# Kernel tuning notes

Measured on AMD Instinct MI355X. Metric: run time of the kernel, lower is better.

Reference implementation:

```python
import jax, jax.numpy as jnp
import numpy as np

D_MODEL = 1024
N_HEADS = 16
HEAD_DIM = D_MODEL // N_HEADS  # 64
TOP_K = 64
EPS = 1e-12  # matches F.normalize eps


def setup_inputs() -> dict:
    key = jax.random.key(0)
    ks = jax.random.split(key, 6)
    s = 0.02
    def w(k):
        return jax.random.normal(k, (D_MODEL, D_MODEL), jnp.float32) * s
    zb = jnp.zeros((D_MODEL,), jnp.float32)
    # x: (B, T, d_model); T must equal d_model (see compress_proj constraint)
    x = jax.random.normal(ks[0], (2, 1024, D_MODEL), jnp.float32)
    return {
        "x": x,
        "Wq": w(ks[1]), "bq": zb,
        "Wk": w(ks[2]), "bk": zb,
        "Wv": w(ks[3]), "bv": zb,
        "Wo": w(ks[4]), "bo": zb,
        "Wc": w(ks[5]), "bc": zb,  # compress_proj (applied along time axis)
    }


def _l2norm(a):
    n = jnp.linalg.norm(a, axis=-1, keepdims=True)
    return a / jnp.maximum(n, EPS)


def reference(x, Wq, bq, Wk, bk, Wv, bv, Wo, bo, Wc, bc):
    B, T, Dm = x.shape
    H, hd = N_HEADS, HEAD_DIM

    def proj(W, b):
        return (x @ W.T + b).reshape(B, T, H, hd).transpose(0, 2, 1, 3)  # (B,H,T,hd)

    Q = proj(Wq, bq)
    K = proj(Wk, bk)
    V = proj(Wv, bv)

    # compress_kv with compress_ratio=1: compress_proj acts on the (transposed)
    # time axis, so K_comp[b,h,c,d] = sum_t K[b,h,t,d] * Wc[c,t] + bc[c]
    K_comp = jnp.einsum('bhtd,ct->bhcd', K, Wc) + bc[None, None, :, None]
    V_comp = jnp.einsum('bhtd,ct->bhcd', V, Wc) + bc[None, None, :, None]

    # lightning indexer: cosine similarity + top-k over compressed slots
    sim = jnp.einsum('bhtd,bhcd->bhtc', _l2norm(Q), _l2norm(K_comp))
    topk_idx = jax.lax.top_k(sim, TOP_K)[1]  # (B,H,T,K)

    bi = jnp.arange(B)[:, None, None, None]
    hi = jnp.arange(H)[None, :, None, None]
    K_sel = K_comp[bi, hi, topk_idx]  # (B,H,T,K,hd)
    V_sel = V_comp[bi, hi, topk_idx]

    scores = jnp.einsum('bhtd,bhtkd->bhtk', Q, K_sel) / float(np.sqrt(hd))
    attn = jax.nn.softmax(scores, axis=-1)
    out = jnp.einsum('bhtk,bhtkd->bhtd', attn, V_sel)  # (B,H,T,hd)
    out = out.transpose(0, 2, 1, 3).reshape(B, T, Dm)
    return out @ Wo.T + bo
```

## Files before the change

kernel.cpp:

```cpp
#include <hip/hip_runtime.h>
#include <type_traits>


#define DEVI __device__ __forceinline__

constexpr int Tn = 1024;
constexpr int Cn = 1024;
constexpr int Hn = 16;

typedef short bf16x8 __attribute__((ext_vector_type(8)));
typedef float f32x4 __attribute__((ext_vector_type(4)));
typedef double f64x4 __attribute__((ext_vector_type(4)));

DEVI int wsumi(int v)   { for (int m = 1; m < 64; m <<= 1) v += __shfl_xor(v, m); return v; }
DEVI int wmini(int v)   { for (int m = 1; m < 64; m <<= 1) { int o = __shfl_xor(v, m); v = o < v ? o : v; } return v; }
DEVI float wfmax(float v){ for (int m = 1; m < 64; m <<= 1) v = fmaxf(v, __shfl_xor(v, m)); return v; }
DEVI float wfsum(float v){ for (int m = 1; m < 64; m <<= 1) v += __shfl_xor(v, m); return v; }

DEVI unsigned long long mapd(double x) {
  unsigned long long b = (unsigned long long)__double_as_longlong(x);
  return (b >> 63) ? ~b : (b | 0x8000000000000000ull);
}

DEVI unsigned short f2bf_rne(float x) {
  unsigned u = __float_as_uint(x);
  u += 0x7fffu + ((u >> 16) & 1u);
  return (unsigned short)(u >> 16);
}
struct BfPair { short hi, lo; };
DEVI BfPair split2(float x) {
  unsigned short h = f2bf_rne(x);
  float hf = __uint_as_float(((unsigned)h) << 16);
  BfPair r;
  r.hi = (short)h;
  r.lo = (short)f2bf_rne(x - hf);
  return r;
}

template <typename OUTT, bool BTRANS, int BIASMODE, bool SIM>
__global__ __launch_bounds__(256) void f64sel_k(
    const float* __restrict__ A, const float* __restrict__ B,
    const float* __restrict__ bias, OUTT* __restrict__ C,
    int Kd, int lda, int ldb, int ldc,
    long long zB, long long zC, int group_base)
{
  __shared__ float As[32][72];
  __shared__ float Bs[32][72];

  size_t offA = 0, offB = 0, offC = 0;
  if (SIM) {
    int pair = group_base + (int)blockIdx.z;
    int bb = pair >> 4, hh = pair & 15;
    offA = ((size_t)bb * Tn) * (size_t)lda + (size_t)hh * 64;
    offB = ((size_t)bb * Cn) * (size_t)ldb + (size_t)hh * 64;
    offC = (size_t)blockIdx.z * (size_t)Tn * (size_t)ldc;
  } else {
    offB = (size_t)blockIdx.z * (size_t)zB;
    offC = (size_t)blockIdx.z * (size_t)zC;
  }
  const float* Ab = A + offA;
  const float* Bb = B + offB;
  OUTT* Cb = C + offC;

  const int tid = threadIdx.x;
  const int lane = tid & 63, w = tid >> 6;
  const int wr = w >> 1, wc = w & 1;
  const int l15 = lane & 15, l4 = lane >> 4;
  const int m0 = blockIdx.y * 64, n0 = blockIdx.x * 64;

  f64x4 zz = {0.0, 0.0, 0.0, 0.0};
  f64x4 p1 = __builtin_amdgcn_mfma_f64_16x16x4f64(1.0, (double)l15, zz, 0, 0, 0);
  f64x4 p2 = __builtin_amdgcn_mfma_f64_16x16x4f64((double)l15, 1.0, zz, 0, 0, 0);
  int a1 = 1, b1 = 1, c1 = 1, a2 = 1, b2 = 1, c2 = 1;
#pragma unroll
  for (int rr = 0; rr < 4; ++rr) {
    a1 &= (p1[rr] == 4.0 * l15);
    b1 &= (p1[rr] == 4.0 * (l4 * 4 + rr));
    c1 &= (p1[rr] == 4.0 * (l4 + 4 * rr));
    a2 &= (p2[rr] == 4.0 * (l4 * 4 + rr));
    b2 &= (p2[rr] == 4.0 * (l4 + 4 * rr));
    c2 &= (p2[rr] == 4.0 * l15);
  }
  a1 = __all(a1); b1 = __all(b1); c1 = __all(c1);
  a2 = __all(a2); b2 = __all(b2); c2 = __all(c2);
  int dmap = 0, useM = 1;
  if      (a1 && a2) dmap = 0;
  else if (a1 && b2) dmap = 1;
  else if (b1 && c2) dmap = 2;
  else if (c1 && c2) dmap = 3;
  else useM = 0;

  f64x4 acc[2][2];
#pragma unroll
  for (int i = 0; i < 2; ++i)
#pragma unroll
    for (int j = 0; j < 2; ++j) acc[i][j] = (f64x4){0.0, 0.0, 0.0, 0.0};

  const int sm = tid >> 2, skf = tid & 3;
  const int bkl = tid >> 4, bnf = tid & 15;

  const int nT = Kd >> 5;
  float4 a0_, a1_, b0_, b1_;
  {
    a0_ = *(const float4*)(Ab + (size_t)(m0 + sm) * lda + 4 * skf);
    a1_ = *(const float4*)(Ab + (size_t)(m0 + sm) * lda + 16 + 4 * skf);
    if (BTRANS) {
      b0_ = *(const float4*)(Bb + (size_t)(n0 + sm) * ldb + 4 * skf);
      b1_ = *(const float4*)(Bb + (size_t)(n0 + sm) * ldb + 16 + 4 * skf);
    } else {
      b0_ = *(const float4*)(Bb + (size_t)bkl * ldb + n0 + 4 * bnf);
      b1_ = *(const float4*)(Bb + (size_t)(16 + bkl) * ldb + n0 + 4 * bnf);
    }
  }

  for (int kt = 0; kt < nT; ++kt) {
    As[4 * skf + 0][sm] = a0_.x; As[4 * skf + 1][sm] = a0_.y;
    As[4 * skf + 2][sm] = a0_.z; As[4 * skf + 3][sm] = a0_.w;
    As[16 + 4 * skf + 0][sm] = a1_.x; As[16 + 4 * skf + 1][sm] = a1_.y;
    As[16 + 4 * skf + 2][sm] = a1_.z; As[16 + 4 * skf + 3][sm] = a1_.w;
    if (BTRANS) {
      Bs[4 * skf + 0][sm] = b0_.x; Bs[4 * skf + 1][sm] = b0_.y;
      Bs[4 * skf + 2][sm] = b0_.z; Bs[4 * skf + 3][sm] = b0_.w;
      Bs[16 + 4 * skf + 0][sm] = b1_.x; Bs[16 + 4 * skf + 1][sm] = b1_.y;
      Bs[16 + 4 * skf + 2][sm] = b1_.z; Bs[16 + 4 * skf + 3][sm] = b1_.w;
    } else {
      *(float4*)&Bs[bkl][4 * bnf] = b0_;
      *(float4*)&Bs[16 + bkl][4 * bnf] = b1_;
    }
    __syncthreads();

    if (kt + 1 < nT) {
      int k0 = (kt + 1) * 32;
      a0_ = *(const float4*)(Ab + (size_t)(m0 + sm) * lda + k0 + 4 * skf);
      a1_ = *(const float4*)(Ab + (size_t)(m0 + sm) * lda + k0 + 16 + 4 * skf);
      if (BTRANS) {
        b0_ = *(const float4*)(Bb + (size_t)(n0 + sm) * ldb + k0 + 4 * skf);
        b1_ = *(const float4*)(Bb + (size_t)(n0 + sm) * ldb + k0 + 16 + 4 * skf);
      } else {
        b0_ = *(const float4*)(Bb + (size_t)(k0 + bkl) * ldb + n0 + 4 * bnf);
        b1_ = *(const float4*)(Bb + (size_t)(k0 + 16 + bkl) * ldb + n0 + 4 * bnf);
      }
    }

    if (useM) {
#pragma unroll
      for (int kq = 0; kq < 8; ++kq) {
        int kk = kq * 4 + l4;
        double a0  = (double)As[kk][wr * 32 + l15];
        double a1v = (double)As[kk][wr * 32 + 16 + l15];
        double b0  = (double)Bs[kk][wc * 32 + l15];
        double b1v = (double)Bs[kk][wc * 32 + 16 + l15];
        acc[0][0] = __builtin_amdgcn_mfma_f64_16x16x4f64(a0,  b0,  acc[0][0], 0, 0, 0);
        acc[0][1] = __builtin_amdgcn_mfma_f64_16x16x4f64(a0,  b1v, acc[0][1], 0, 0, 0);
        acc[1][0] = __builtin_amdgcn_mfma_f64_16x16x4f64(a1v, b0,  acc[1][0], 0, 0, 0);
        acc[1][1] = __builtin_amdgcn_mfma_f64_16x16x4f64(a1v, b1v, acc[1][1], 0, 0, 0);
      }
    } else {
#pragma unroll
      for (int k = 0; k < 32; ++k) {
        double bv0 = (double)Bs[k][wc * 32 + l15];
        double bv1 = (double)Bs[k][wc * 32 + 16 + l15];
#pragma unroll
        for (int fr = 0; fr < 2; ++fr)
#pragma unroll
          for (int rr = 0; rr < 4; ++rr) {
            double av = (double)As[k][wr * 32 + fr * 16 + l4 * 4 + rr];
            acc[fr][0][rr] += av * bv0;
            acc[fr][1][rr] += av * bv1;
          }
      }
    }
    __syncthreads();
  }

#pragma unroll
  for (int fr = 0; fr < 2; ++fr)
#pragma unroll
    for (int fc = 0; fc < 2; ++fc)
#pragma unroll
      for (int rr = 0; rr < 4; ++rr) {
        int ri, ci;
        if (!useM || dmap == 0) { ri = l4 * 4 + rr; ci = l15; }
        else if (dmap == 1)     { ri = l4 + 4 * rr; ci = l15; }
        else if (dmap == 2)     { ri = l15; ci = l4 * 4 + rr; }
        else                    { ri = l15; ci = l4 + 4 * rr; }
        int row = m0 + wr * 32 + fr * 16 + ri;
        int col = n0 + wc * 32 + fc * 16 + ci;
        double v = acc[fr][fc][rr];
        if constexpr (std::is_same<OUTT, double>::value) {
          Cb[(size_t)row * ldc + col] = v;
        } else {
          float s = (float)v;
          float cb = (BIASMODE == 1) ? bias[col] : 0.f;
          float rb = (BIASMODE == 2) ? bias[row] : 0.f;
          ((float*)Cb)[(size_t)row * ldc + col] = s + cb + rb;
        }
      }
}

template <bool BTRANS, int BIASMODE>
__global__ __launch_bounds__(256) void mfma_gemm_k(
    const float* __restrict__ A, const float* __restrict__ B,
    const float* __restrict__ bias, float* __restrict__ C,
    int Kd, int lda, int ldb, int ldc, long long zB, long long zC)
{
  __shared__ short Ah[4 * 64 * 8];
  __shared__ short Al[4 * 64 * 8];
  __shared__ short Bh[4 * 64 * 8];
  __shared__ short Bl[4 * 64 * 8];

  const float* Bz = B + (size_t)blockIdx.z * (size_t)zB;
  float* Cz = C + (size_t)blockIdx.z * (size_t)zC;

  const int tid = threadIdx.x;
  const int lane = tid & 63, w = tid >> 6;
  const int wr = w >> 1, wc = w & 1;
  const int m0 = blockIdx.y * 64, n0 = blockIdx.x * 64;
  const int r16 = lane & 15, kg = lane >> 4;

  f32x4 acc[2][2];
#pragma unroll
  for (int i = 0; i < 2; ++i)
#pragma unroll
    for (int j = 0; j < 2; ++j) acc[i][j] = (f32x4){0.f, 0.f, 0.f, 0.f};

  const int row = tid >> 2, kseg = tid & 3;
  const int gcol = tid & 63, gks = tid >> 6;

  const int nT = Kd >> 5;
  float4 pa0, pa1, pb0, pb1;
  float gb[8];
  {
    pa0 = *(const float4*)(A + (size_t)(m0 + row) * lda + kseg * 8);
    pa1 = *(const float4*)(A + (size_t)(m0 + row) * lda + kseg * 8 + 4);
    if (BTRANS) {
      pb0 = *(const float4*)(Bz + (size_t)(n0 + row) * ldb + kseg * 8);
      pb1 = *(const float4*)(Bz + (size_t)(n0 + row) * ldb + kseg * 8 + 4);
    } else {
#pragma unroll
      for (int j = 0; j < 8; ++j)
        gb[j] = Bz[(size_t)(gks * 8 + j) * ldb + n0 + gcol];
    }
  }

  for (int kt = 0; kt < nT; ++kt) {
    {
      BfPair q0 = split2(pa0.x), q1 = split2(pa0.y), q2 = split2(pa0.z), q3 = split2(pa0.w);
      BfPair q4 = split2(pa1.x), q5 = split2(pa1.y), q6 = split2(pa1.z), q7 = split2(pa1.w);
      bf16x8 h = {q0.hi, q1.hi, q2.hi, q3.hi, q4.hi, q5.hi, q6.hi, q7.hi};
      bf16x8 l = {q0.lo, q1.lo, q2.lo, q3.lo, q4.lo, q5.lo, q6.lo, q7.lo};
      int idx = (kseg * 64 + row) * 8;
      *(bf16x8*)&Ah[idx] = h;
      *(bf16x8*)&Al[idx] = l;
    }
    if (BTRANS) {
      BfPair q0 = split2(pb0.x), q1 = split2(pb0.y), q2 = split2(pb0.z), q3 = split2(pb0.w);
      BfPair q4 = split2(pb1.x), q5 = split2(pb1.y), q6 = split2(pb1.z), q7 = split2(pb1.w);
      bf16x8 h = {q0.hi, q1.hi, q2.hi, q3.hi, q4.hi, q5.hi, q6.hi, q7.hi};
      bf16x8 l = {q0.lo, q1.lo, q2.lo, q3.lo, q4.lo, q5.lo, q6.lo, q7.lo};
      int idx = (kseg * 64 + row) * 8;
      *(bf16x8*)&Bh[idx] = h;
      *(bf16x8*)&Bl[idx] = l;
    } else {
      short hv[8], lv[8];
#pragma unroll
      for (int j = 0; j < 8; ++j) {
        BfPair p = split2(gb[j]);
        hv[j] = p.hi; lv[j] = p.lo;
      }
      bf16x8 h = {hv[0], hv[1], hv[2], hv[3], hv[4], hv[5], hv[6], hv[7]};
      bf16x8 l = {lv[0], lv[1], lv[2], lv[3], lv[4], lv[5], lv[6], lv[7]};
      int idx = (gks * 64 + gcol) * 8;
      *(bf16x8*)&Bh[idx] = h;
      *(bf16x8*)&Bl[idx] = l;
    }
    __syncthreads();

    if (kt + 1 < nT) {
      int k0 = (kt + 1) * 32;
      pa0 = *(const float4*)(A + (size_t)(m0 + row) * lda + k0 + kseg * 8);
      pa1 = *(const float4*)(A + (size_t)(m0 + row) * lda + k0 + kseg * 8 + 4);
      if (BTRANS) {
        pb0 = *(const float4*)(Bz + (size_t)(n0 + row) * ldb + k0 + kseg * 8);
        pb1 = *(const float4*)(Bz + (size_t)(n0 + row) * ldb + k0 + kseg * 8 + 4);
      } else {
#pragma unroll
        for (int j = 0; j < 8; ++j)
          gb[j] = Bz[(size_t)(k0 + gks * 8 + j) * ldb + n0 + gcol];
      }
    }

    bf16x8 ah[2], al[2], bh[2], bl[2];
#pragma unroll
    for (int f = 0; f < 2; ++f) {
      int ia = (kg * 64 + wr * 32 + f * 16 + r16) * 8;
      int ib = (kg * 64 + wc * 32 + f * 16 + r16) * 8;
      ah[f] = *(const bf16x8*)&Ah[ia];
      al[f] = *(const bf16x8*)&Al[ia];
      bh[f] = *(const bf16x8*)&Bh[ib];
      bl[f] = *(const bf16x8*)&Bl[ib];
    }
#pragma unroll
    for (int fr = 0; fr < 2; ++fr)
#pragma unroll
      for (int fc = 0; fc < 2; ++fc) {
        f32x4 c = acc[fr][fc];
        c = __builtin_amdgcn_mfma_f32_16x16x32_bf16(al[fr], bh[fc], c, 0, 0, 0);
        c = __builtin_amdgcn_mfma_f32_16x16x32_bf16(ah[fr], bl[fc], c, 0, 0, 0);
        c = __builtin_amdgcn_mfma_f32_16x16x32_bf16(ah[fr], bh[fc], c, 0, 0, 0);
        acc[fr][fc] = c;
      }
    __syncthreads();
  }

#pragma unroll
  for (int fr = 0; fr < 2; ++fr)
#pragma unroll
    for (int fc = 0; fc < 2; ++fc) {
      int col = n0 + wc * 32 + fc * 16 + r16;
      float cb = (BIASMODE == 1) ? bias[col] : 0.f;
#pragma unroll
      for (int rr = 0; rr < 4; ++rr) {
        int rw = m0 + wr * 32 + fr * 16 + kg * 4 + rr;
        float rb = (BIASMODE == 2) ? bias[rw] : 0.f;
        Cz[(size_t)rw * ldc + col] = acc[fr][fc][rr] + cb + rb;
      }
    }
}

__global__ __launch_bounds__(256) void kn_k2(const float* __restrict__ Kc,
                                             double* __restrict__ kn)
{
  int idx = (int)blockIdx.x * 256 + (int)threadIdx.x;
  int c = idx & 1023;
  int p = idx >> 10;
  int b = p >> 4, h = p & 15;
  const float* row = Kc + ((size_t)(b * 1024 + c)) * 1024 + h * 64;
  double s = 0.0;
  for (int d = 0; d < 64; ++d) { double v = (double)row[d]; s += v * v; }
  kn[(size_t)p * 1024 + c] = 1.0 / fmax(sqrt(s), 1e-12);
}

__global__ __launch_bounds__(256) void topk_attn_k(
    const double* __restrict__ dotb, const double* __restrict__ kn,
    const float* __restrict__ Vc, float* __restrict__ attnout, int group_base)
{
  __shared__ int sC[4][64];
  __shared__ float sD[4][64];

  const int lane = threadIdx.x & 63, wv = threadIdx.x >> 6;
  const int g = (int)blockIdx.x >> 8;
  const int t = ((int)blockIdx.x & 255) * 4 + wv;
  const int pair = group_base + g;
  const int bb = pair >> 4, hh = pair & 15;

  const double* drow = dotb + ((size_t)g * Tn + t) * (size_t)Cn;
  const double* knr  = kn + ((size_t)(bb * Hn + hh)) * Cn;

  double dv[16];
  unsigned long long u[16];
#pragma unroll
  for (int j = 0; j < 8; ++j) {
    double2 dd = *(const double2*)(drow + j * 128 + 2 * lane);
    double2 kk = *(const double2*)(knr  + j * 128 + 2 * lane);
    dv[2 * j] = dd.x; dv[2 * j + 1] = dd.y;
    u[2 * j]     = mapd(dd.x * kk.x);
    u[2 * j + 1] = mapd(dd.y * kk.y);
  }
  unsigned hi[16];
#pragma unroll
  for (int i = 0; i < 16; ++i) hi[i] = (unsigned)(u[i] >> 32);

  unsigned TH = 0;
  for (int bit = 31; bit >= 0; --bit) {
    unsigned Tc = TH | (1u << bit);
    int c = 0;
#pragma unroll
    for (int i = 0; i < 16; ++i) c += (hi[i] >= Tc);
    if (wsumi(c) >= 64) TH = Tc;
  }
  int mhi = 0;
#pragma unroll
  for (int i = 0; i < 16; ++i) mhi += (hi[i] > TH);
  mhi = wsumi(mhi);
  const int need1 = 64 - mhi;
  unsigned TL = 0;
  for (int bit = 31; bit >= 0; --bit) {
    unsigned Tc = TL | (1u << bit);
    int c = 0;
#pragma unroll
    for (int i = 0; i < 16; ++i) c += (hi[i] == TH && (unsigned)u[i] >= Tc);
    if (wsumi(c) >= need1) TL = Tc;
  }
  const unsigned long long V64 = ((unsigned long long)TH << 32) | TL;

  int base = 0;
#pragma unroll
  for (int i = 0; i < 16; ++i) {
    const int cix = 128 * (i >> 1) + 2 * lane + (i & 1);
    bool sel = (u[i] > V64);
    unsigned long long mk = __ballot(sel);
    if (sel) {
      int r = __popcll(mk & ((1ull << lane) - 1ull));
      sC[wv][base + r] = cix;
      sD[wv][base + r] = (float)dv[i];
    }
    base += __popcll(mk);
  }
  const int need = 64 - base;
  unsigned taken = 0;
  for (int r = 0; r < need; ++r) {
    int mn = 0x7fffffff;
#pragma unroll
    for (int i = 0; i < 16; ++i) {
      int cix = 128 * (i >> 1) + 2 * lane + (i & 1);
      if (u[i] == V64 && !((taken >> i) & 1u)) mn = mn < cix ? mn : cix;
    }
    mn = wmini(mn);
#pragma unroll
    for (int i = 0; i < 16; ++i) {
      int cix = 128 * (i >> 1) + 2 * lane + (i & 1);
      if (u[i] == V64 && !((taken >> i) & 1u) && cix == mn) {
        taken |= 1u << i;
        sC[wv][base + r] = mn;
        sD[wv][base + r] = (float)dv[i];
      }
    }
  }
  __syncthreads();

  int ck = sC[wv][lane];
  float sc = sD[wv][lane] * 0.125f;
  float mx = wfmax(sc);
  float w = expf(sc - mx);
  float sw = wfsum(w);
  w /= sw;

  const float* Vb = Vc + (size_t)bb * ((size_t)Cn * 1024) + hh * 64 + lane;
  float acc = 0.f;
#pragma unroll 4
  for (int k = 0; k < 64; ++k) {
    int c = __shfl(ck, k);
    float wk = __shfl(w, k);
    acc = fmaf(wk, Vb[(size_t)c * 1024], acc);
  }
  attnout[((size_t)(bb * Tn + t)) * 1024 + hh * 64 + lane] = acc;
}

extern "C" void kernel_launch(void* const* d_in, const int* in_sizes, int n_in,
                              void* d_out, int out_size, void* d_ws, size_t ws_size,
                              hipStream_t stream)
{
  const float* x  = (const float*)d_in[0];
  const float* Wq = (const float*)d_in[1];
  const float* bq = (const float*)d_in[2];
  const float* Wk = (const float*)d_in[3];
  const float* bk = (const float*)d_in[4];
  const float* Wv = (const float*)d_in[5];
  const float* bv = (const float*)d_in[6];
  const float* Wo = (const float*)d_in[7];
  const float* bo = (const float*)d_in[8];
  const float* Wc = (const float*)d_in[9];
  const float* bc = (const float*)d_in[10];
  float* out = (float*)d_out;

  const size_t NE = (size_t)2048 * 1024;
  const size_t M1 = (size_t)1024 * 1024;
  float* Q   = (float*)d_ws;
  float* Kf  = Q + NE;
  float* Vf  = Kf + NE;
  float* Kc  = Vf + NE;
  float* Vc  = Kc + NE;
  float* at  = Vc + NE;
  double* kn = (double*)(at + NE);
  double* tail = kn + 32768;

  const size_t fixedB = 6 * NE * 4 + 32768 * 8;
  const size_t dotPairB = (size_t)Tn * Cn * 8;
  if (ws_size < fixedB) return;

  size_t rem = ws_size - fixedB;
  double* dotp; int G;
  if      (rem >= 8 * dotPairB) { G = 8; dotp = tail; }
  else if (rem >= 4 * dotPairB) { G = 4; dotp = tail; }
  else if (rem >= 2 * dotPairB) { G = 2; dotp = tail; }
  else { G = 2; dotp = (double*)Kf; }

  dim3 blk(256, 1, 1);

  f64sel_k<float, true, 1, false><<<dim3(16, 32, 1), blk, 0, stream>>>(
      x, Wq, bq, Q, 1024, 1024, 1024, 1024, 0, 0, 0);
  f64sel_k<float, true, 1, false><<<dim3(16, 32, 1), blk, 0, stream>>>(
      x, Wk, bk, Kf, 1024, 1024, 1024, 1024, 0, 0, 0);
  mfma_gemm_k<true, 1><<<dim3(16, 32, 1), blk, 0, stream>>>(
      x, Wv, bv, Vf, 1024, 1024, 1024, 1024, 0, 0);

  f64sel_k<float, false, 2, false><<<dim3(16, 16, 2), blk, 0, stream>>>(
      Wc, Kf, bc, Kc, 1024, 1024, 1024, 1024, (long long)M1, (long long)M1, 0);
  mfma_gemm_k<false, 2><<<dim3(16, 16, 2), blk, 0, stream>>>(
      Wc, Vf, bc, Vc, 1024, 1024, 1024, 1024, (long long)M1, (long long)M1);

  kn_k2<<<dim3(128), blk, 0, stream>>>(Kc, kn);

  for (int gb = 0; gb < 32; gb += G) {
    f64sel_k<double, true, 0, true><<<dim3(16, 16, G), blk, 0, stream>>>(
        Q, Kc, nullptr, dotp, 64, 1024, 1024, 1024, 0, 0, gb);
    topk_attn_k<<<dim3(256 * G), blk, 0, stream>>>(dotp, kn, Vc, at, gb);
  }

  mfma_gemm_k<true, 1><<<dim3(16, 32, 1), blk, 0, stream>>>(
      at, Wo, bo, out, 1024, 1024, 1024, 1024, 0, 0);
}
```

Measured before the change: 856.8 us.

## Double-buffer GEMM LDS tiles, batch Q/K projections, enlarge similarity group size

Both GEMM kernels now use two shared-memory buffers. The next tile is written to the idle buffer after the compute step, so each k-iteration needs one barrier instead of two. The Q and K projections are merged into a single launch through a new mode that picks weights, bias and output from blockIdx.z. The similarity/top-k group size can now reach 32 pairs when the workspace allows, which cuts the number of launch pairs. In exchange, LDS use doubles, which may lower occupancy, and the larger groups need more workspace.

```diff
diff --git a/kernel.cpp b/kernel.cpp
--- a/kernel.cpp
+++ b/kernel.cpp
@@ -37,30 +37,32 @@
   return r;
 }
 
-template <typename OUTT, bool BTRANS, int BIASMODE, bool SIM>
+template <typename OUTT, bool BTRANS, int BIASMODE, int MODE>
 __global__ __launch_bounds__(256) void f64sel_k(
     const float* __restrict__ A, const float* __restrict__ B,
-    const float* __restrict__ bias, OUTT* __restrict__ C,
+    const float* __restrict__ Bx, const float* __restrict__ bias,
+    const float* __restrict__ biasx, OUTT* __restrict__ C, OUTT* __restrict__ Cx,
     int Kd, int lda, int ldb, int ldc,
     long long zB, long long zC, int group_base)
 {
-  __shared__ float As[32][72];
-  __shared__ float Bs[32][72];
-
-  size_t offA = 0, offB = 0, offC = 0;
-  if (SIM) {
+  __shared__ float As[2][32][72];
+  __shared__ float Bs[2][32][72];
+
+  const float* Ab = A;
+  const float* Bb = B;
+  OUTT* Cb = C;
+  if (MODE == 1) {
     int pair = group_base + (int)blockIdx.z;
     int bb = pair >> 4, hh = pair & 15;
-    offA = ((size_t)bb * Tn) * (size_t)lda + (size_t)hh * 64;
-    offB = ((size_t)bb * Cn) * (size_t)ldb + (size_t)hh * 64;
-    offC = (size_t)blockIdx.z * (size_t)Tn * (size_t)ldc;
+    Ab = A + ((size_t)bb * Tn) * (size_t)lda + (size_t)hh * 64;
+    Bb = B + ((size_t)bb * Cn) * (size_t)ldb + (size_t)hh * 64;
+    Cb = C + (size_t)blockIdx.z * (size_t)Tn * (size_t)ldc;
+  } else if (MODE == 0) {
+    Bb = B + (size_t)blockIdx.z * (size_t)zB;
+    Cb = C + (size_t)blockIdx.z * (size_t)zC;
   } else {
-    offB = (size_t)blockIdx.z * (size_t)zB;
-    offC = (size_t)blockIdx.z * (size_t)zC;
-  }
-  const float* Ab = A + offA;
-  const float* Bb = B + offB;
-  OUTT* Cb = C + offC;
+    if (blockIdx.z == 1) { Bb = Bx; bias = biasx; Cb = Cx; }
+  }
 
   const int tid = threadIdx.x;
   const int lane = tid & 63, w = tid >> 6;
@@ -101,55 +103,50 @@
 
   const int nT = Kd >> 5;
   float4 a0_, a1_, b0_, b1_;
-  {
-    a0_ = *(const float4*)(Ab + (size_t)(m0 + sm) * lda + 4 * skf);
-    a1_ = *(const float4*)(Ab + (size_t)(m0 + sm) * lda + 16 + 4 * skf);
+
+  auto LOADT = [&](int k0) {
+    a0_ = *(const float4*)(Ab + (size_t)(m0 + sm) * lda + k0 + 4 * skf);
+    a1_ = *(const float4*)(Ab + (size_t)(m0 + sm) * lda + k0 + 16 + 4 * skf);
     if (BTRANS) {
-      b0_ = *(const float4*)(Bb + (size_t)(n0 + sm) * ldb + 4 * skf);
-      b1_ = *(const float4*)(Bb + (size_t)(n0 + sm) * ldb + 16 + 4 * skf);
+      b0_ = *(const float4*)(Bb + (size_t)(n0 + sm) * ldb + k0 + 4 * skf);
+      b1_ = *(const float4*)(Bb + (size_t)(n0 + sm) * ldb + k0 + 16 + 4 * skf);
     } else {
-      b0_ = *(const float4*)(Bb + (size_t)bkl * ldb + n0 + 4 * bnf);
-      b1_ = *(const float4*)(Bb + (size_t)(16 + bkl) * ldb + n0 + 4 * bnf);
-    }
-  }
+      b0_ = *(const float4*)(Bb + (size_t)(k0 + bkl) * ldb + n0 + 4 * bnf);
+      b1_ = *(const float4*)(Bb + (size_t)(k0 + 16 + bkl) * ldb + n0 + 4 * bnf);
+    }
+  };
+  auto WRITET = [&](int buf) {
+    As[buf][4 * skf + 0][sm] = a0_.x; As[buf][4 * skf + 1][sm] = a0_.y;
+    As[buf][4 * skf + 2][sm] = a0_.z; As[buf][4 * skf + 3][sm] = a0_.w;
+    As[buf][16 + 4 * skf + 0][sm] = a1_.x; As[buf][16 + 4 * skf + 1][sm] = a1_.y;
+    As[buf][16 + 4 * skf + 2][sm] = a1_.z; As[buf][16 + 4 * skf + 3][sm] = a1_.w;
+    if (BTRANS) {
+      Bs[buf][4 * skf + 0][sm] = b0_.x; Bs[buf][4 * skf + 1][sm] = b0_.y;
+      Bs[buf][4 * skf + 2][sm] = b0_.z; Bs[buf][4 * skf + 3][sm] = b0_.w;
+      Bs[buf][16 + 4 * skf + 0][sm] = b1_.x; Bs[buf][16 + 4 * skf + 1][sm] = b1_.y;
+      Bs[buf][16 + 4 * skf + 2][sm] = b1_.z; Bs[buf][16 + 4 * skf + 3][sm] = b1_.w;
+    } else {
+      *(float4*)&Bs[buf][bkl][4 * bnf] = b0_;
+      *(float4*)&Bs[buf][16 + bkl][4 * bnf] = b1_;
+    }
+  };
+
+  LOADT(0);
+  WRITET(0);
+  __syncthreads();
 
   for (int kt = 0; kt < nT; ++kt) {
-    As[4 * skf + 0][sm] = a0_.x; As[4 * skf + 1][sm] = a0_.y;
-    As[4 * skf + 2][sm] = a0_.z; As[4 * skf + 3][sm] = a0_.w;
-    As[16 + 4 * skf + 0][sm] = a1_.x; As[16 + 4 * skf + 1][sm] = a1_.y;
-    As[16 + 4 * skf + 2][sm] = a1_.z; As[16 + 4 * skf + 3][sm] = a1_.w;
-    if (BTRANS) {
-      Bs[4 * skf + 0][sm] = b0_.x; Bs[4 * skf + 1][sm] = b0_.y;
-      Bs[4 * skf + 2][sm] = b0_.z; Bs[4 * skf + 3][sm] = b0_.w;
-      Bs[16 + 4 * skf + 0][sm] = b1_.x; Bs[16 + 4 * skf + 1][sm] = b1_.y;
-      Bs[16 + 4 * skf + 2][sm] = b1_.z; Bs[16 + 4 * skf + 3][sm] = b1_.w;
-    } else {
-      *(float4*)&Bs[bkl][4 * bnf] = b0_;
-      *(float4*)&Bs[16 + bkl][4 * bnf] = b1_;
-    }
-    __syncthreads();
-
-    if (kt + 1 < nT) {
-      int k0 = (kt + 1) * 32;
-      a0_ = *(const float4*)(Ab + (size_t)(m0 + sm) * lda + k0 + 4 * skf);
-      a1_ = *(const float4*)(Ab + (size_t)(m0 + sm) * lda + k0 + 16 + 4 * skf);
-      if (BTRANS) {
-        b0_ = *(const float4*)(Bb + (size_t)(n0 + sm) * ldb + k0 + 4 * skf);
-        b1_ = *(const float4*)(Bb + (size_t)(n0 + sm) * ldb + k0 + 16 + 4 * skf);
-      } else {
-        b0_ = *(const float4*)(Bb + (size_t)(k0 + bkl) * ldb + n0 + 4 * bnf);
-        b1_ = *(const float4*)(Bb + (size_t)(k0 + 16 + bkl) * ldb + n0 + 4 * bnf);
-      }
-    }
+    const int cur = kt & 1;
+    if (kt + 1 < nT) LOADT((kt + 1) * 32);
 
     if (useM) {
 #pragma unroll
       for (int kq = 0; kq < 8; ++kq) {
         int kk = kq * 4 + l4;
-        double a0  = (double)As[kk][wr * 32 + l15];
-        double a1v = (double)As[kk][wr * 32 + 16 + l15];
-        double b0  = (double)Bs[kk][wc * 32 + l15];
-        double b1v = (double)Bs[kk][wc * 32 + 16 + l15];
+        double a0  = (double)As[cur][kk][wr * 32 + l15];
+        double a1v = (double)As[cur][kk][wr * 32 + 16 + l15];
+        double b0  = (double)Bs[cur][kk][wc * 32 + l15];
+        double b1v = (double)Bs[cur][kk][wc * 32 + 16 + l15];
         acc[0][0] = __builtin_amdgcn_mfma_f64_16x16x4f64(a0,  b0,  acc[0][0], 0, 0, 0);
         acc[0][1] = __builtin_amdgcn_mfma_f64_16x16x4f64(a0,  b1v, acc[0][1], 0, 0, 0);
         acc[1][0] = __builtin_amdgcn_mfma_f64_16x16x4f64(a1v, b0,  acc[1][0], 0, 0, 0);
@@ -158,18 +155,20 @@
     } else {
 #pragma unroll
       for (int k = 0; k < 32; ++k) {
-        double bv0 = (double)Bs[k][wc * 32 + l15];
-        double bv1 = (double)Bs[k][wc * 32 + 16 + l15];
+        double bv0 = (double)Bs[cur][k][wc * 32 + l15];
+        double bv1 = (double)Bs[cur][k][wc * 32 + 16 + l15];
 #pragma unroll
         for (int fr = 0; fr < 2; ++fr)
 #pragma unroll
           for (int rr = 0; rr < 4; ++rr) {
-            double av = (double)As[k][wr * 32 + fr * 16 + l4 * 4 + rr];
+            double av = (double)As[cur][k][wr * 32 + fr * 16 + l4 * 4 + rr];
             acc[fr][0][rr] += av * bv0;
             acc[fr][1][rr] += av * bv1;
           }
       }
     }
+
+    if (kt + 1 < nT) WRITET(cur ^ 1);
     __syncthreads();
   }
 
@@ -204,10 +203,10 @@
     const float* __restrict__ bias, float* __restrict__ C,
     int Kd, int lda, int ldb, int ldc, long long zB, long long zC)
 {
-  __shared__ short Ah[4 * 64 * 8];
-  __shared__ short Al[4 * 64 * 8];
-  __shared__ short Bh[4 * 64 * 8];
-  __shared__ short Bl[4 * 64 * 8];
+  __shared__ short Ah[2][4 * 64 * 8];
+  __shared__ short Al[2][4 * 64 * 8];
+  __shared__ short Bh[2][4 * 64 * 8];
+  __shared__ short Bl[2][4 * 64 * 8];
 
   const float* Bz = B + (size_t)blockIdx.z * (size_t)zB;
   float* Cz = C + (size_t)blockIdx.z * (size_t)zC;
@@ -230,28 +229,28 @@
   const int nT = Kd >> 5;
   float4 pa0, pa1, pb0, pb1;
   float gb[8];
-  {
-    pa0 = *(const float4*)(A + (size_t)(m0 + row) * lda + kseg * 8);
-    pa1 = *(const float4*)(A + (size_t)(m0 + row) * lda + kseg * 8 + 4);
+
+  auto LOADT = [&](int k0) {
+    pa0 = *(const float4*)(A + (size_t)(m0 + row) * lda + k0 + kseg * 8);
+    pa1 = *(const float4*)(A + (size_t)(m0 + row) * lda + k0 + kseg * 8 + 4);
     if (BTRANS) {
-      pb0 = *(const float4*)(Bz + (size_t)(n0 + row) * ldb + kseg * 8);
-      pb1 = *(const float4*)(Bz + (size_t)(n0 + row) * ldb + kseg * 8 + 4);
+      pb0 = *(const float4*)(Bz + (size_t)(n0 + row) * ldb + k0 + kseg * 8);
+      pb1 = *(const float4*)(Bz + (size_t)(n0 + row) * ldb + k0 + kseg * 8 + 4);
     } else {
 #pragma unroll
       for (int j = 0; j < 8; ++j)
-        gb[j] = Bz[(size_t)(gks * 8 + j) * ldb + n0 + gcol];
-    }
-  }
-
-  for (int kt = 0; kt < nT; ++kt) {
+        gb[j] = Bz[(size_t)(k0 + gks * 8 + j) * ldb + n0 + gcol];
+    }
+  };
+  auto WRITET = [&](int buf) {
     {
       BfPair q0 = split2(pa0.x), q1 = split2(pa0.y), q2 = split2(pa0.z), q3 = split2(pa0.w);
       BfPair q4 = split2(pa1.x), q5 = split2(pa1.y), q6 = split2(pa1.z), q7 = split2(pa1.w);
       bf16x8 h = {q0.hi, q1.hi, q2.hi, q3.hi, q4.hi, q5.hi, q6.hi, q7.hi};
       bf16x8 l = {q0.lo, q1.lo, q2.lo, q3.lo, q4.lo, q5.lo, q6.lo, q7.lo};
       int idx = (kseg * 64 + row) * 8;
-      *(bf16x8*)&Ah[idx] = h;
-      *(bf16x8*)&Al[idx] = l;
+      *(bf16x8*)&Ah[buf][idx] = h;
+      *(bf16x8*)&Al[buf][idx] = l;
     }
     if (BTRANS) {
       BfPair q0 = split2(pb0.x), q1 = split2(pb0.y), q2 = split2(pb0.z), q3 = split2(pb0.w);
@@ -259,8 +258,8 @@
       bf16x8 h = {q0.hi, q1.hi, q2.hi, q3.hi, q4.hi, q5.hi, q6.hi, q7.hi};
       bf16x8 l = {q0.lo, q1.lo, q2.lo, q3.lo, q4.lo, q5.lo, q6.lo, q7.lo};
       int idx = (kseg * 64 + row) * 8;
-      *(bf16x8*)&Bh[idx] = h;
-      *(bf16x8*)&Bl[idx] = l;
+      *(bf16x8*)&Bh[buf][idx] = h;
+      *(bf16x8*)&Bl[buf][idx] = l;
     } else {
       short hv[8], lv[8];
 #pragma unroll
@@ -271,34 +270,28 @@
       bf16x8 h = {hv[0], hv[1], hv[2], hv[3], hv[4], hv[5], hv[6], hv[7]};
       bf16x8 l = {lv[0], lv[1], lv[2], lv[3], lv[4], lv[5], lv[6], lv[7]};
       int idx = (gks * 64 + gcol) * 8;
-      *(bf16x8*)&Bh[idx] = h;
-      *(bf16x8*)&Bl[idx] = l;
-    }
-    __syncthreads();
-
-    if (kt + 1 < nT) {
-      int k0 = (kt + 1) * 32;
-      pa0 = *(const float4*)(A + (size_t)(m0 + row) * lda + k0 + kseg * 8);
-      pa1 = *(const float4*)(A + (size_t)(m0 + row) * lda + k0 + kseg * 8 + 4);
-      if (BTRANS) {
-        pb0 = *(const float4*)(Bz + (size_t)(n0 + row) * ldb + k0 + kseg * 8);
-        pb1 = *(const float4*)(Bz + (size_t)(n0 + row) * ldb + k0 + kseg * 8 + 4);
-      } else {
-#pragma unroll
-        for (int j = 0; j < 8; ++j)
-          gb[j] = Bz[(size_t)(k0 + gks * 8 + j) * ldb + n0 + gcol];
-      }
-    }
+      *(bf16x8*)&Bh[buf][idx] = h;
+      *(bf16x8*)&Bl[buf][idx] = l;
+    }
+  };
+
+  LOADT(0);
+  WRITET(0);
+  __syncthreads();
+
+  for (int kt = 0; kt < nT; ++kt) {
+    const int cur = kt & 1;
+    if (kt + 1 < nT) LOADT((kt + 1) * 32);
 
     bf16x8 ah[2], al[2], bh[2], bl[2];
 #pragma unroll
     for (int f = 0; f < 2; ++f) {
       int ia = (kg * 64 + wr * 32 + f * 16 + r16) * 8;
       int ib = (kg * 64 + wc * 32 + f * 16 + r16) * 8;
-      ah[f] = *(const bf16x8*)&Ah[ia];
-      al[f] = *(const bf16x8*)&Al[ia];
-      bh[f] = *(const bf16x8*)&Bh[ib];
-      bl[f] = *(const bf16x8*)&Bl[ib];
+      ah[f] = *(const bf16x8*)&Ah[cur][ia];
+      al[f] = *(const bf16x8*)&Al[cur][ia];
+      bh[f] = *(const bf16x8*)&Bh[cur][ib];
+      bl[f] = *(const bf16x8*)&Bl[cur][ib];
     }
 #pragma unroll
     for (int fr = 0; fr < 2; ++fr)
@@ -310,6 +303,8 @@
         c = __builtin_amdgcn_mfma_f32_16x16x32_bf16(ah[fr], bh[fc], c, 0, 0, 0);
         acc[fr][fc] = c;
       }
+
+    if (kt + 1 < nT) WRITET(cur ^ 1);
     __syncthreads();
   }
 
@@ -481,30 +476,32 @@
 
   size_t rem = ws_size - fixedB;
   double* dotp; int G;
-  if      (rem >= 8 * dotPairB) { G = 8; dotp = tail; }
-  else if (rem >= 4 * dotPairB) { G = 4; dotp = tail; }
-  else if (rem >= 2 * dotPairB) { G = 2; dotp = tail; }
+  if      (rem >= 32 * dotPairB) { G = 32; dotp = tail; }
+  else if (rem >= 16 * dotPairB) { G = 16; dotp = tail; }
+  else if (rem >=  8 * dotPairB) { G = 8;  dotp = tail; }
+  else if (rem >=  4 * dotPairB) { G = 4;  dotp = tail; }
+  else if (rem >=  2 * dotPairB) { G = 2;  dotp = tail; }
   else { G = 2; dotp = (double*)Kf; }
 
   dim3 blk(256, 1, 1);
 
-  f64sel_k<float, true, 1, false><<<dim3(16, 32, 1), blk, 0, stream>>>(
-      x, Wq, bq, Q, 1024, 1024, 1024, 1024, 0, 0, 0);
-  f64sel_k<float, true, 1, false><<<dim3(16, 32, 1), blk, 0, stream>>>(
-      x, Wk, bk, Kf, 1024, 1024, 1024, 1024, 0, 0, 0);
+  f64sel_k<float, true, 1, 2><<<dim3(16, 32, 2), blk, 0, stream>>>(
+      x, Wq, Wk, bq, bk, Q, Kf, 1024, 1024, 1024, 1024, 0, 0, 0);
   mfma_gemm_k<true, 1><<<dim3(16, 32, 1), blk, 0, stream>>>(
       x, Wv, bv, Vf, 1024, 1024, 1024, 1024, 0, 0);
 
-  f64sel_k<float, false, 2, false><<<dim3(16, 16, 2), blk, 0, stream>>>(
-      Wc, Kf, bc, Kc, 1024, 1024, 1024, 1024, (long long)M1, (long long)M1, 0);
+  f64sel_k<float, false, 2, 0><<<dim3(16, 16, 2), blk, 0, stream>>>(
+      Wc, Kf, nullptr, bc, nullptr, Kc, nullptr,
+      1024, 1024, 1024, 1024, (long long)M1, (long long)M1, 0);
   mfma_gemm_k<false, 2><<<dim3(16, 16, 2), blk, 0, stream>>>(
       Wc, Vf, bc, Vc, 1024, 1024, 1024, 1024, (long long)M1, (long long)M1);
 
   kn_k2<<<dim3(128), blk, 0, stream>>>(Kc, kn);
 
   for (int gb = 0; gb < 32; gb += G) {
-    f64sel_k<double, true, 0, true><<<dim3(16, 16, G), blk, 0, stream>>>(
-        Q, Kc, nullptr, dotp, 64, 1024, 1024, 1024, 0, 0, gb);
+    f64sel_k<double, true, 0, 1><<<dim3(16, 16, G), blk, 0, stream>>>(
+        Q, Kc, nullptr, nullptr, nullptr, dotp, nullptr,
+        64, 1024, 1024, 1024, 0, 0, gb);
     topk_attn_k<<<dim3(256 * G), blk, 0, stream>>>(dotp, kn, Vc, at, gb);
   }
 
```

Result: faster. 812.5 us (-5.2%).
